# Optimization experiments

Measured on AMD Instinct MI355X. Metric: run time of the kernel, lower is better.

The kernel has to match this reference:

```python
import jax, jax.numpy as jnp
import numpy as np

DIM = 1024
NUM_HEADS = 16
HEAD_DIM = DIM // NUM_HEADS
SCALE = HEAD_DIM ** -0.5


def setup_inputs() -> dict:
    key = jax.random.key(0)
    ks = jax.random.split(key, 11)
    B, N, M = 8, 1024, 1024
    s = DIM ** -0.5  # init scale for weights
    return {
        "x": jax.random.normal(ks[0], (B, N, DIM), jnp.float32),
        "context": jax.random.normal(ks[1], (B, M, DIM), jnp.float32),
        "Wq": jax.random.normal(ks[2], (DIM, DIM), jnp.float32) * s,
        "bq": jax.random.normal(ks[3], (DIM,), jnp.float32) * 0.01,
        "Wk": jax.random.normal(ks[4], (DIM, DIM), jnp.float32) * s,
        "bk": jax.random.normal(ks[5], (DIM,), jnp.float32) * 0.01,
        "Wv": jax.random.normal(ks[6], (DIM, DIM), jnp.float32) * s,
        "bv": jax.random.normal(ks[7], (DIM,), jnp.float32) * 0.01,
        "Wo": jax.random.normal(ks[8], (DIM, DIM), jnp.float32) * s,
        "bo": jax.random.normal(ks[9], (DIM,), jnp.float32) * 0.01,
    }


def reference(x, context, Wq, bq, Wk, bk, Wv, bv, Wo, bo):
    B, N, _ = x.shape
    M = context.shape[1]
    # Linear projections (torch Linear: x @ W.T + b; here W stored as [in, out])
    q = x @ Wq + bq            # [B, N, DIM]
    k = context @ Wk + bk      # [B, M, DIM]
    v = context @ Wv + bv      # [B, M, DIM]
    # split heads: b n (h d) -> b h n d
    q = q.reshape(B, N, NUM_HEADS, HEAD_DIM).transpose(0, 2, 1, 3)
    k = k.reshape(B, M, NUM_HEADS, HEAD_DIM).transpose(0, 2, 1, 3)
    v = v.reshape(B, M, NUM_HEADS, HEAD_DIM).transpose(0, 2, 1, 3)
    dots = jnp.einsum('bhnd,bhmd->bhnm', q, k) * SCALE
    attn = jax.nn.softmax(dots, axis=-1)
    out = jnp.einsum('bhnm,bhmd->bhnd', attn, v)   # [B, H, N, d]
    out = out.transpose(0, 2, 1, 3).reshape(B, N, DIM)  # b h n d -> b n (h d)
    return out @ Wo + bo
```

## Files before the change

kernel.cpp:

```cpp
#include <hip/hip_runtime.h>

typedef unsigned short u16;
typedef __attribute__((ext_vector_type(8))) short bf16x8;
typedef __attribute__((ext_vector_type(4))) float f32x4;
typedef __attribute__((ext_vector_type(16))) float f32x16;
typedef __attribute__((ext_vector_type(4))) unsigned u32x4;

#define MFMA16 __builtin_amdgcn_mfma_f32_16x16x32_bf16
#define MFMA32 __builtin_amdgcn_mfma_f32_32x32x16_bf16

__device__ __forceinline__ u16 f2b(float f) {
  unsigned u = __builtin_bit_cast(unsigned, f);
  u = (u + 0x7fffu + ((u >> 16) & 1u)) >> 16;
  return (u16)u;
}

__device__ __forceinline__ void gload_lds16(const u16* g, u16* l) {
  __builtin_amdgcn_global_load_lds((const __attribute__((address_space(1))) void*)g,
                                   (__attribute__((address_space(3))) void*)l, 16, 0, 0);
}

__global__ void prep(const float* __restrict__ x, const float* __restrict__ ctx,
                     u16* __restrict__ xb, u16* __restrict__ cb,
                     const float* __restrict__ w0, const float* __restrict__ w1,
                     const float* __restrict__ w2, const float* __restrict__ w3,
                     u16* __restrict__ o0, u16* __restrict__ o1,
                     u16* __restrict__ o2, u16* __restrict__ o3) {
  __shared__ float t[64][65];
  const int z = blockIdx.z;
  const int tid = threadIdx.x;
  if (z < 2) {
    int i = blockIdx.x * blockDim.x + tid;
    const float* in = z ? ctx : x;
    u16* out = z ? cb : xb;
    float4 v = reinterpret_cast<const float4*>(in)[i];
    reinterpret_cast<ushort4*>(out)[i] = make_ushort4(f2b(v.x), f2b(v.y), f2b(v.z), f2b(v.w));
    return;
  }
  const int id = blockIdx.x;
  if (id >= 1024) return;
  const int wsel = id >> 8;
  const float* src = wsel == 0 ? w0 : wsel == 1 ? w1 : wsel == 2 ? w2 : w3;
  u16* dst = wsel == 0 ? o0 : wsel == 1 ? o1 : wsel == 2 ? o2 : o3;
  const int r0 = ((id >> 4) & 15) * 64, c0 = (id & 15) * 64;
  #pragma unroll
  for (int it = 0; it < 4; ++it) {
    int row = it * 16 + (tid >> 4);
    int col = (tid & 15) * 4;
    float4 v = *reinterpret_cast<const float4*>(&src[(size_t)(r0 + row) * 1024 + c0 + col]);
    t[row][col] = v.x; t[row][col + 1] = v.y; t[row][col + 2] = v.z; t[row][col + 3] = v.w;
  }
  __syncthreads();
  #pragma unroll
  for (int it = 0; it < 2; ++it) {
    int c = it * 32 + (tid >> 3);
    int r8 = (tid & 7) * 8;
    u16 tmp[8];
    #pragma unroll
    for (int k = 0; k < 8; ++k) tmp[k] = f2b(t[r8 + k][c]);
    uint4 pk;
    pk.x = (unsigned)tmp[0] | ((unsigned)tmp[1] << 16);
    pk.y = (unsigned)tmp[2] | ((unsigned)tmp[3] << 16);
    pk.z = (unsigned)tmp[4] | ((unsigned)tmp[5] << 16);
    pk.w = (unsigned)tmp[6] | ((unsigned)tmp[7] << 16);
    *reinterpret_cast<uint4*>(&dst[(size_t)(c0 + c) * 1024 + r0 + r8]) = pk;
  }
}

__global__ __launch_bounds__(512, 2) void gemm_qkv256(
    const u16* __restrict__ xb, const u16* __restrict__ cb,
    const u16* __restrict__ Wqt, const u16* __restrict__ Wkt, const u16* __restrict__ Wvt,
    const float* __restrict__ bq, const float* __restrict__ bk, const float* __restrict__ bv,
    u16* __restrict__ Qb, u16* __restrict__ Kf, u16* __restrict__ Vf) {
  __shared__ u16 smem[65536];
  const int tid = threadIdx.x;
  const int lane = tid & 63;
  const int w = tid >> 6;
  const int wr = w >> 2, wc = w & 3;
  const int l16 = lane & 15, g = (lane >> 4) & 3;
  const int z = blockIdx.z;
  const u16* Ain = z == 0 ? xb : cb;
  const u16* W = z == 0 ? Wqt : z == 1 ? Wkt : Wvt;
  const float* bias = z == 0 ? bq : z == 1 ? bk : bv;
  const int brow = blockIdx.x * 256, bcol = blockIdx.y * 256;

  int aoff[4], boff[4];
  #pragma unroll
  for (int it = 0; it < 4; ++it) {
    const int c = it * 512 + tid;
    const int kk = ((c >> 6) & 1) * 32 + ((c >> 4) & 3) * 8;
    const int arow = (c >> 10) * 128 + ((c >> 7) & 7) * 16 + (c & 15);
    aoff[it] = (brow + arow) * 1024 + kk;
    const int bcolc = (c >> 9) * 64 + ((c >> 7) & 3) * 16 + (c & 15);
    boff[it] = (bcol + bcolc) * 1024 + kk;
  }
  auto stage = [&](int buf, int t) {
    u16* db = smem + buf * 32768;
    #pragma unroll
    for (int it = 0; it < 4; ++it)
      gload_lds16(&Ain[(size_t)(aoff[it] + t * 64)], db + (it * 512 + w * 64) * 8);
    #pragma unroll
    for (int it = 0; it < 4; ++it)
      gload_lds16(&W[(size_t)(boff[it] + t * 64)], db + 16384 + (it * 512 + w * 64) * 8);
  };

  f32x4 acc[8][4] = {};
  stage(0, 0);
  stage(1, 1);
  asm volatile("s_waitcnt vmcnt(8)" ::: "memory");
  __builtin_amdgcn_sched_barrier(0);
  __builtin_amdgcn_s_barrier();
  __builtin_amdgcn_sched_barrier(0);

  for (int t = 0; t < 16; ++t) {
    const int cur = t & 1;
    const u16* As = smem + cur * 32768;
    const u16* Bs = As + 16384;
    bf16x8 bfr[2][4];
    #pragma unroll
    for (int ks = 0; ks < 2; ++ks)
      #pragma unroll
      for (int ni = 0; ni < 4; ++ni)
        bfr[ks][ni] = *reinterpret_cast<const bf16x8*>(&Bs[(wc * 512 + ni * 128 + ks * 64 + lane) * 8]);
    __builtin_amdgcn_s_setprio(1);
    #pragma unroll
    for (int mi = 0; mi < 8; ++mi) {
      bf16x8 a0 = *reinterpret_cast<const bf16x8*>(&As[(wr * 1024 + mi * 128 + lane) * 8]);
      bf16x8 a1 = *reinterpret_cast<const bf16x8*>(&As[(wr * 1024 + mi * 128 + 64 + lane) * 8]);
      #pragma unroll
      for (int ni = 0; ni < 4; ++ni)
        acc[mi][ni] = MFMA16(a1, bfr[1][ni], MFMA16(a0, bfr[0][ni], acc[mi][ni], 0, 0, 0), 0, 0, 0);
    }
    __builtin_amdgcn_s_setprio(0);
    __builtin_amdgcn_sched_barrier(0);
    __builtin_amdgcn_s_barrier();
    __builtin_amdgcn_sched_barrier(0);
    if (t < 14) {
      stage(cur, t + 2);
      asm volatile("s_waitcnt vmcnt(8)" ::: "memory");
    } else {
      asm volatile("s_waitcnt vmcnt(0)" ::: "memory");
    }
    __builtin_amdgcn_sched_barrier(0);
    __builtin_amdgcn_s_barrier();
    __builtin_amdgcn_sched_barrier(0);
  }

  u16* T = smem + w * 4608;
  float bz[4];
  #pragma unroll
  for (int ni = 0; ni < 4; ++ni) bz[ni] = bias[bcol + wc * 64 + ni * 16 + l16];
  const float CS = 0.125f * 1.44269504089f;
  const int h = (bcol + wc * 64) >> 6;
  #pragma unroll
  for (int p = 0; p < 2; ++p) {
    if (z < 2) {
      #pragma unroll
      for (int mi4 = 0; mi4 < 4; ++mi4)
        #pragma unroll
        for (int ni = 0; ni < 4; ++ni) {
          f32x4 v = acc[p * 4 + mi4][ni];
          #pragma unroll
          for (int j = 0; j < 4; ++j) {
            float val = v[j] + bz[ni];
            if (z == 0) val *= CS;
            T[(mi4 * 16 + g * 4 + j) * 72 + ni * 16 + l16] = f2b(val);
          }
        }
      if (z == 0) {
        #pragma unroll
        for (int it = 0; it < 8; ++it) {
          const int rl = it * 8 + (lane >> 3), c8 = (lane & 7) * 8;
          bf16x8 val = *reinterpret_cast<const bf16x8*>(&T[rl * 72 + c8]);
          *reinterpret_cast<bf16x8*>(
              &Qb[(size_t)(brow + wr * 128 + p * 64 + rl) * 1024 + bcol + wc * 64 + c8]) = val;
        }
      } else {
        #pragma unroll
        for (int it = 0; it < 8; ++it) {
          const int rl = it * 8 + (lane >> 3), c8 = (lane & 7) * 8;
          bf16x8 val = *reinterpret_cast<const bf16x8*>(&T[rl * 72 + c8]);
          const int m = brow + wr * 128 + p * 64 + rl;
          const int bb = m >> 10, kt = (m & 1023) >> 6;
          const int chunk = (c8 >> 4) * 128 + ((m & 63) >> 5) * 64 + ((c8 >> 3) & 1) * 32 + (m & 31);
          *reinterpret_cast<bf16x8*>(&Kf[(((size_t)(bb * 16 + h)) * 16 + kt) * 4096 + chunk * 8]) = val;
        }
      }
    } else {
      #pragma unroll
      for (int mi4 = 0; mi4 < 4; ++mi4)
        #pragma unroll
        for (int ni = 0; ni < 4; ++ni) {
          f32x4 v = acc[p * 4 + mi4][ni];
          #pragma unroll
          for (int j = 0; j < 4; ++j)
            T[(ni * 16 + l16) * 72 + mi4 * 16 + g * 4 + j] = f2b(v[j] + bz[ni]);
        }
      #pragma unroll
      for (int it = 0; it < 8; ++it) {
        const int d = it * 8 + (lane >> 3), m8 = (lane & 7) * 8;
        bf16x8 val = *reinterpret_cast<const bf16x8*>(&T[d * 72 + m8]);
        const int m = brow + wr * 128 + p * 64 + m8;
        const int bb = m >> 10, kt = (m & 1023) >> 6;
        const int chunk = (m8 >> 4) * 128 + (d >> 5) * 64 + ((m8 >> 3) & 1) * 32 + (d & 31);
        *reinterpret_cast<bf16x8*>(&Vf[(((size_t)(bb * 16 + h)) * 16 + kt) * 4096 + chunk * 8]) = val;
      }
    }
  }
}

__device__ __forceinline__ void gemm_core(const u16* __restrict__ A, const u16* __restrict__ Wt,
                                          f32x4 (&acc)[4][4], int brow, int bcol,
                                          u16* __restrict__ smem) {
  const int tid = threadIdx.x;
  const int lane = tid & 63;
  const int w = tid >> 6;
  const int wr = w >> 1, wc = w & 1;
  const int l16 = lane & 15, g = lane >> 4;

  auto stage = [&](int buf, int kt) {
    #pragma unroll
    for (int it = 0; it < 4; ++it) {
      int c = it * 256 + tid;
      int row = (c >> 2) & 127;
      int ks = c >> 9;
      int k8 = c & 3;
      const size_t gofs = (size_t)kt * 64 + ks * 32 + k8 * 8;
      gload_lds16(&A[(size_t)(brow + row) * 1024 + gofs],
                  &smem[buf * 8192 + (it * 256 + w * 64) * 8]);
      gload_lds16(&Wt[(size_t)(bcol + row) * 1024 + gofs],
                  &smem[16384 + buf * 8192 + (it * 256 + w * 64) * 8]);
    }
  };

  stage(0, 0);
  __syncthreads();
  int cur = 0;
  for (int kt = 0; kt < 16; ++kt) {
    if (kt < 15) stage(cur ^ 1, kt + 1);
    const u16* As = &smem[cur * 8192];
    const u16* Bs = &smem[16384 + cur * 8192];
    #pragma unroll
    for (int ks = 0; ks < 2; ++ks) {
      bf16x8 a[4], b[4];
      const int kb = ks * 4096 + g * 8;
      #pragma unroll
      for (int mi = 0; mi < 4; ++mi)
        a[mi] = *reinterpret_cast<const bf16x8*>(&As[kb + (wr * 64 + mi * 16 + l16) * 32]);
      #pragma unroll
      for (int ni = 0; ni < 4; ++ni)
        b[ni] = *reinterpret_cast<const bf16x8*>(&Bs[kb + (wc * 64 + ni * 16 + l16) * 32]);
      #pragma unroll
      for (int mi = 0; mi < 4; ++mi)
        #pragma unroll
        for (int ni = 0; ni < 4; ++ni)
          acc[mi][ni] = MFMA16(a[mi], b[ni], acc[mi][ni], 0, 0, 0);
    }
    __syncthreads();
    cur ^= 1;
  }
}

__global__ __launch_bounds__(256, 2) void gemm_o(const u16* __restrict__ A, const u16* __restrict__ Wt,
                                                 const float* __restrict__ bias, float* __restrict__ outp) {
  __shared__ u16 smem[32768];
  const int brow = blockIdx.x * 128, bcol = blockIdx.y * 128;
  f32x4 acc[4][4] = {};
  gemm_core(A, Wt, acc, brow, bcol, smem);
  const int lane = threadIdx.x & 63;
  const int w = threadIdx.x >> 6;
  const int wr = w >> 1, wc = w & 1;
  const int l16 = lane & 15, g = lane >> 4;
  #pragma unroll
  for (int ni = 0; ni < 4; ++ni) {
    const int col = bcol + wc * 64 + ni * 16 + l16;
    const float bz = bias[col];
    #pragma unroll
    for (int mi = 0; mi < 4; ++mi) {
      const int r0 = brow + wr * 64 + mi * 16 + g * 4;
      f32x4 v = acc[mi][ni];
      #pragma unroll
      for (int j = 0; j < 4; ++j) outp[(size_t)(r0 + j) * 1024 + col] = v[j] + bz;
    }
  }
}

__global__ __launch_bounds__(256, 2) void attn2(const u16* __restrict__ Q, const u16* __restrict__ Kf,
                                                const u16* __restrict__ Vf, u16* __restrict__ AO) {
  __shared__ u16 Ks[2][64 * 64];
  __shared__ u16 Vs[2][64 * 64];
  const int tid = threadIdx.x, lane = tid & 63, w = tid >> 6;
  const int l32 = lane & 31, u = lane >> 5;
  const int id = blockIdx.x;
  const int v = (id & 7) * 128 + (id >> 3);
  const int qt = v & 7, h = (v >> 3) & 15, b = v >> 7;
  const int q0 = qt * 128 + w * 32;

  bf16x8 qf[4];
  {
    const u16* qp = &Q[(size_t)(b * 1024 + q0 + l32) * 1024 + h * 64 + u * 8];
    #pragma unroll
    for (int m = 0; m < 4; ++m) qf[m] = *reinterpret_cast<const bf16x8*>(qp + m * 16);
  }

  f32x16 o0 = {}, o1 = {};
  float lr = 0.f;

  const u16* Kbh = Kf + (size_t)(b * 16 + h) * 65536;
  const u16* Vbh = Vf + (size_t)(b * 16 + h) * 65536;

  auto stage = [&](int buf, int kt) {
    #pragma unroll
    for (int it = 0; it < 2; ++it) {
      const int c = (it * 256 + tid) * 8;
      gload_lds16(&Kbh[kt * 4096 + c], &Ks[buf][(it * 256 + w * 64) * 8]);
      gload_lds16(&Vbh[kt * 4096 + c], &Vs[buf][(it * 256 + w * 64) * 8]);
    }
  };

  stage(0, 0);
  __syncthreads();
  int cur = 0;

  for (int kt = 0; kt < 16; ++kt) {
    if (kt < 15) stage(cur ^ 1, kt + 1);

    f32x16 s0 = {}, s1 = {};
    __builtin_amdgcn_s_setprio(1);
    #pragma unroll
    for (int m = 0; m < 4; ++m) {
      bf16x8 k0 = *reinterpret_cast<const bf16x8*>(&Ks[cur][m * 1024 + lane * 8]);
      bf16x8 k1 = *reinterpret_cast<const bf16x8*>(&Ks[cur][m * 1024 + 512 + lane * 8]);
      s0 = MFMA32(k0, qf[m], s0, 0, 0, 0);
      s1 = MFMA32(k1, qf[m], s1, 0, 0, 0);
    }
    __builtin_amdgcn_s_setprio(0);

    unsigned W0[8], W1[8];
    #pragma unroll
    for (int j = 0; j < 8; ++j) {
      const int r = 4 * (j >> 1) + 2 * (j & 1);
      float pa0 = __builtin_amdgcn_exp2f(s0[r]);
      float pb0 = __builtin_amdgcn_exp2f(s0[r + 1]);
      float pa1 = __builtin_amdgcn_exp2f(s1[r]);
      float pb1 = __builtin_amdgcn_exp2f(s1[r + 1]);
      lr += (pa0 + pb0) + (pa1 + pb1);
      asm("v_cvt_pk_bf16_f32 %0, %1, %2" : "=v"(W0[j]) : "v"(pa0), "v"(pb0));
      asm("v_cvt_pk_bf16_f32 %0, %1, %2" : "=v"(W1[j]) : "v"(pa1), "v"(pb1));
    }

    unsigned paw[4][4];
    #pragma unroll
    for (int ks = 0; ks < 4; ++ks) {
      const int ksl = ks & 1;
      #pragma unroll
      for (int p = 0; p < 2; ++p) {
        unsigned x = (ks < 2) ? W0[4 * ksl + p] : W1[4 * ksl + p];
        unsigned y = (ks < 2) ? W0[4 * ksl + 2 + p] : W1[4 * ksl + 2 + p];
        asm("v_permlane32_swap_b32 %0, %1" : "+v"(x), "+v"(y));
        paw[ks][p] = x;
        paw[ks][2 + p] = y;
      }
    }

    __builtin_amdgcn_s_setprio(1);
    #pragma unroll
    for (int ks = 0; ks < 4; ++ks) {
      bf16x8 pa = __builtin_bit_cast(bf16x8, u32x4{paw[ks][0], paw[ks][1], paw[ks][2], paw[ks][3]});
      bf16x8 v0 = *reinterpret_cast<const bf16x8*>(&Vs[cur][ks * 1024 + lane * 8]);
      bf16x8 v1 = *reinterpret_cast<const bf16x8*>(&Vs[cur][ks * 1024 + 512 + lane * 8]);
      o0 = MFMA32(pa, v0, o0, 0, 0, 0);
      o1 = MFMA32(pa, v1, o1, 0, 0, 0);
    }
    __builtin_amdgcn_s_setprio(0);

    __syncthreads();
    cur ^= 1;
  }

  float sum = lr + __shfl_xor(lr, 32);
  float rinv = 1.0f / sum;
  u16* aop = &AO[(size_t)(b * 1024 + q0) * 1024 + h * 64 + l32];
  #pragma unroll
  for (int r = 0; r < 16; ++r) {
    const int ql = (r & 3) + 8 * (r >> 2) + 4 * u;
    int ri_i = __builtin_amdgcn_ds_bpermute((ql + (u << 5)) << 2, __builtin_bit_cast(int, rinv));
    float ri = __builtin_bit_cast(float, ri_i);
    aop[(size_t)ql * 1024] = f2b(o0[r] * ri);
    aop[(size_t)ql * 1024 + 32] = f2b(o1[r] * ri);
  }
}

extern "C" void kernel_launch(void* const* d_in, const int* in_sizes, int n_in,
                              void* d_out, int out_size, void* d_ws, size_t ws_size,
                              hipStream_t stream) {
  const float* x   = (const float*)d_in[0];
  const float* ctx = (const float*)d_in[1];
  const float* Wq  = (const float*)d_in[2];
  const float* bq  = (const float*)d_in[3];
  const float* Wk  = (const float*)d_in[4];
  const float* bk  = (const float*)d_in[5];
  const float* Wv  = (const float*)d_in[6];
  const float* bv  = (const float*)d_in[7];
  const float* Wo  = (const float*)d_in[8];
  const float* bo  = (const float*)d_in[9];
  float* out = (float*)d_out;
  char* ws = (char*)d_ws;

  u16* xb  = (u16*)(ws + (size_t)0);
  u16* cb  = (u16*)(ws + ((size_t)16 << 20));
  u16* Qb  = (u16*)(ws + ((size_t)32 << 20));
  u16* Kf  = (u16*)(ws + ((size_t)48 << 20));
  u16* Vf  = (u16*)(ws + ((size_t)64 << 20));
  u16* Wqt = (u16*)(ws + ((size_t)80 << 20));
  u16* Wkt = (u16*)(ws + ((size_t)82 << 20));
  u16* Wvt = (u16*)(ws + ((size_t)84 << 20));
  u16* Wot = (u16*)(ws + ((size_t)86 << 20));

  prep<<<dim3(8192, 1, 3), 256, 0, stream>>>(x, ctx, xb, cb, Wq, Wk, Wv, Wo, Wqt, Wkt, Wvt, Wot);
  gemm_qkv256<<<dim3(32, 4, 3), 512, 0, stream>>>(xb, cb, Wqt, Wkt, Wvt, bq, bk, bv, Qb, Kf, Vf);
  attn2<<<dim3(1024), 256, 0, stream>>>(Qb, Kf, Vf, xb );
  gemm_o<<<dim3(64, 8), 256, 0, stream>>>(xb, Wot, bo, out);
}
```

Before: 172.5 us.

## Split QKV GEMM K-step into four quadrant phases with finer-grained prefetch

```diff
diff --git a/kernel.cpp b/kernel.cpp
--- a/kernel.cpp
+++ b/kernel.cpp
@@ -67,6 +67,35 @@
   }
 }
 
+#define PHASE(BUF, HA, HB, STAGE, VM)                                            \
+  do {                                                                           \
+    const u16* Ab = smem + (BUF) * 32768 + (HA) * 8192;                          \
+    const u16* Bb = smem + (BUF) * 32768 + 16384 + (HB) * 8192;                  \
+    bf16x8 afr[4][2], bfr[2][2];                                                 \
+    _Pragma("unroll") for (int mil = 0; mil < 4; ++mil)                          \
+      _Pragma("unroll") for (int ks = 0; ks < 2; ++ks)                           \
+        afr[mil][ks] = *(const bf16x8*)&Ab[(wr * 512 + mil * 128 + ks * 64 + lane) * 8]; \
+    _Pragma("unroll") for (int nil = 0; nil < 2; ++nil)                          \
+      _Pragma("unroll") for (int ks = 0; ks < 2; ++ks)                           \
+        bfr[nil][ks] = *(const bf16x8*)&Bb[(wc * 256 + nil * 128 + ks * 64 + lane) * 8]; \
+    STAGE;                                                                       \
+    asm volatile("s_waitcnt vmcnt(" #VM ")" ::: "memory");                       \
+    __builtin_amdgcn_sched_barrier(0);                                           \
+    __builtin_amdgcn_s_barrier();                                                \
+    asm volatile("s_waitcnt lgkmcnt(0)" ::: "memory");                           \
+    __builtin_amdgcn_sched_barrier(0);                                           \
+    __builtin_amdgcn_s_setprio(1);                                               \
+    _Pragma("unroll") for (int mil = 0; mil < 4; ++mil)                          \
+      _Pragma("unroll") for (int nil = 0; nil < 2; ++nil)                        \
+        acc[(HA) * 4 + mil][(HB) * 2 + nil] =                                    \
+            MFMA16(afr[mil][1], bfr[nil][1],                                     \
+                   MFMA16(afr[mil][0], bfr[nil][0],                              \
+                          acc[(HA) * 4 + mil][(HB) * 2 + nil], 0, 0, 0), 0, 0, 0); \
+    __builtin_amdgcn_s_setprio(0);                                               \
+    __builtin_amdgcn_sched_barrier(0);                                           \
+    __builtin_amdgcn_s_barrier();                                                \
+  } while (0)
+
 __global__ __launch_bounds__(512, 2) void gemm_qkv256(
     const u16* __restrict__ xb, const u16* __restrict__ cb,
     const u16* __restrict__ Wqt, const u16* __restrict__ Wkt, const u16* __restrict__ Wvt,
@@ -78,73 +107,59 @@
   const int w = tid >> 6;
   const int wr = w >> 2, wc = w & 3;
   const int l16 = lane & 15, g = (lane >> 4) & 3;
-  const int z = blockIdx.z;
+  const int id = blockIdx.x;
+  const int v = (id & 7) * 48 + (id >> 3);
+  const int bx = v & 31, by = (v >> 5) & 3, z = v >> 7;
   const u16* Ain = z == 0 ? xb : cb;
   const u16* W = z == 0 ? Wqt : z == 1 ? Wkt : Wvt;
   const float* bias = z == 0 ? bq : z == 1 ? bk : bv;
-  const int brow = blockIdx.x * 256, bcol = blockIdx.y * 256;
-
-  int aoff[4], boff[4];
-  #pragma unroll
-  for (int it = 0; it < 4; ++it) {
+  const int brow = bx * 256, bcol = by * 256;
+
+  int aoff0[2], boff0[2];
+  #pragma unroll
+  for (int it = 0; it < 2; ++it) {
     const int c = it * 512 + tid;
     const int kk = ((c >> 6) & 1) * 32 + ((c >> 4) & 3) * 8;
-    const int arow = (c >> 10) * 128 + ((c >> 7) & 7) * 16 + (c & 15);
-    aoff[it] = (brow + arow) * 1024 + kk;
-    const int bcolc = (c >> 9) * 64 + ((c >> 7) & 3) * 16 + (c & 15);
-    boff[it] = (bcol + bcolc) * 1024 + kk;
-  }
-  auto stage = [&](int buf, int t) {
-    u16* db = smem + buf * 32768;
-    #pragma unroll
-    for (int it = 0; it < 4; ++it)
-      gload_lds16(&Ain[(size_t)(aoff[it] + t * 64)], db + (it * 512 + w * 64) * 8);
-    #pragma unroll
-    for (int it = 0; it < 4; ++it)
-      gload_lds16(&W[(size_t)(boff[it] + t * 64)], db + 16384 + (it * 512 + w * 64) * 8);
+    const int arow = ((c >> 9) & 1) * 128 + ((c >> 7) & 3) * 16 + (c & 15);
+    aoff0[it] = (brow + arow) * 1024 + kk;
+    const int bcolc = (c >> 8) * 64 + ((c >> 7) & 1) * 16 + (c & 15);
+    boff0[it] = (bcol + bcolc) * 1024 + kk;
+  }
+  auto stageA = [&](int buf, int h, int kt) {
+    u16* db = smem + buf * 32768 + h * 8192;
+    #pragma unroll
+    for (int it = 0; it < 2; ++it)
+      gload_lds16(&Ain[(size_t)(aoff0[it] + h * 65536 + kt * 64)], db + (it * 512 + w * 64) * 8);
   };
+  auto stageB = [&](int buf, int h, int kt) {
+    u16* db = smem + buf * 32768 + 16384 + h * 8192;
+    #pragma unroll
+    for (int it = 0; it < 2; ++it)
+      gload_lds16(&W[(size_t)(boff0[it] + h * 32768 + kt * 64)], db + (it * 512 + w * 64) * 8);
+  };
 
   f32x4 acc[8][4] = {};
-  stage(0, 0);
-  stage(1, 1);
+  stageA(0, 0, 0); stageB(0, 0, 0); stageB(0, 1, 0); stageA(0, 1, 0);
+  stageA(1, 0, 1); stageB(1, 0, 1);
   asm volatile("s_waitcnt vmcnt(8)" ::: "memory");
   __builtin_amdgcn_sched_barrier(0);
   __builtin_amdgcn_s_barrier();
-  __builtin_amdgcn_sched_barrier(0);
-
-  for (int t = 0; t < 16; ++t) {
-    const int cur = t & 1;
-    const u16* As = smem + cur * 32768;
-    const u16* Bs = As + 16384;
-    bf16x8 bfr[2][4];
-    #pragma unroll
-    for (int ks = 0; ks < 2; ++ks)
-      #pragma unroll
-      for (int ni = 0; ni < 4; ++ni)
-        bfr[ks][ni] = *reinterpret_cast<const bf16x8*>(&Bs[(wc * 512 + ni * 128 + ks * 64 + lane) * 8]);
-    __builtin_amdgcn_s_setprio(1);
-    #pragma unroll
-    for (int mi = 0; mi < 8; ++mi) {
-      bf16x8 a0 = *reinterpret_cast<const bf16x8*>(&As[(wr * 1024 + mi * 128 + lane) * 8]);
-      bf16x8 a1 = *reinterpret_cast<const bf16x8*>(&As[(wr * 1024 + mi * 128 + 64 + lane) * 8]);
-      #pragma unroll
-      for (int ni = 0; ni < 4; ++ni)
-        acc[mi][ni] = MFMA16(a1, bfr[1][ni], MFMA16(a0, bfr[0][ni], acc[mi][ni], 0, 0, 0), 0, 0, 0);
-    }
-    __builtin_amdgcn_s_setprio(0);
-    __builtin_amdgcn_sched_barrier(0);
-    __builtin_amdgcn_s_barrier();
-    __builtin_amdgcn_sched_barrier(0);
-    if (t < 14) {
-      stage(cur, t + 2);
-      asm volatile("s_waitcnt vmcnt(8)" ::: "memory");
-    } else {
-      asm volatile("s_waitcnt vmcnt(0)" ::: "memory");
-    }
-    __builtin_amdgcn_sched_barrier(0);
-    __builtin_amdgcn_s_barrier();
-    __builtin_amdgcn_sched_barrier(0);
-  }
+
+  for (int t = 0; t < 14; ++t) {
+    const int buf = t & 1;
+    PHASE(buf, 0, 0, stageB(buf ^ 1, 1, t + 1), 8);
+    PHASE(buf, 0, 1, stageA(buf ^ 1, 1, t + 1), 8);
+    PHASE(buf, 1, 0, stageA(buf, 0, t + 2), 8);
+    PHASE(buf, 1, 1, stageB(buf, 0, t + 2), 8);
+  }
+  PHASE(0, 0, 0, stageB(1, 1, 15), 8);
+  PHASE(0, 0, 1, stageA(1, 1, 15), 8);
+  PHASE(0, 1, 0, ((void)0), 8);
+  PHASE(0, 1, 1, ((void)0), 4);
+  PHASE(1, 0, 0, ((void)0), 2);
+  PHASE(1, 0, 1, ((void)0), 0);
+  PHASE(1, 1, 0, ((void)0), 0);
+  PHASE(1, 1, 1, ((void)0), 0);
 
   u16* T = smem + w * 4608;
   float bz[4];
@@ -159,10 +174,10 @@
       for (int mi4 = 0; mi4 < 4; ++mi4)
         #pragma unroll
         for (int ni = 0; ni < 4; ++ni) {
-          f32x4 v = acc[p * 4 + mi4][ni];
+          f32x4 vv = acc[p * 4 + mi4][ni];
           #pragma unroll
           for (int j = 0; j < 4; ++j) {
-            float val = v[j] + bz[ni];
+            float val = vv[j] + bz[ni];
             if (z == 0) val *= CS;
             T[(mi4 * 16 + g * 4 + j) * 72 + ni * 16 + l16] = f2b(val);
           }
@@ -191,10 +206,10 @@
       for (int mi4 = 0; mi4 < 4; ++mi4)
         #pragma unroll
         for (int ni = 0; ni < 4; ++ni) {
-          f32x4 v = acc[p * 4 + mi4][ni];
+          f32x4 vv = acc[p * 4 + mi4][ni];
           #pragma unroll
           for (int j = 0; j < 4; ++j)
-            T[(ni * 16 + l16) * 72 + mi4 * 16 + g * 4 + j] = f2b(v[j] + bz[ni]);
+            T[(ni * 16 + l16) * 72 + mi4 * 16 + g * 4 + j] = f2b(vv[j] + bz[ni]);
         }
       #pragma unroll
       for (int it = 0; it < 8; ++it) {
@@ -418,7 +433,7 @@
   u16* Wot = (u16*)(ws + ((size_t)86 << 20));
 
   prep<<<dim3(8192, 1, 3), 256, 0, stream>>>(x, ctx, xb, cb, Wq, Wk, Wv, Wo, Wqt, Wkt, Wvt, Wot);
-  gemm_qkv256<<<dim3(32, 4, 3), 512, 0, stream>>>(xb, cb, Wqt, Wkt, Wvt, bq, bk, bv, Qb, Kf, Vf);
+  gemm_qkv256<<<dim3(384), 512, 0, stream>>>(xb, cb, Wqt, Wkt, Wvt, bq, bk, bv, Qb, Kf, Vf);
   attn2<<<dim3(1024), 256, 0, stream>>>(Qb, Kf, Vf, xb );
   gemm_o<<<dim3(64, 8), 256, 0, stream>>>(xb, Wot, bo, out);
 }
```

After: 166.5 us. 1.04x faster.

## Restructure QKV GEMM pipeline to issue next-tile loads before compute with one barrier

Applied to the files above, without the earlier changes.

```diff
diff --git a/kernel.cpp b/kernel.cpp
--- a/kernel.cpp
+++ b/kernel.cpp
@@ -80,7 +80,7 @@
   const int l16 = lane & 15, g = (lane >> 4) & 3;
   const int z = blockIdx.z;
   const u16* Ain = z == 0 ? xb : cb;
-  const u16* W = z == 0 ? Wqt : z == 1 ? Wkt : Wvt;
+  const u16* Wt = z == 0 ? Wqt : z == 1 ? Wkt : Wvt;
   const float* bias = z == 0 ? bq : z == 1 ? bk : bv;
   const int brow = blockIdx.x * 256, bcol = blockIdx.y * 256;
 
@@ -88,62 +88,56 @@
   #pragma unroll
   for (int it = 0; it < 4; ++it) {
     const int c = it * 512 + tid;
-    const int kk = ((c >> 6) & 1) * 32 + ((c >> 4) & 3) * 8;
-    const int arow = (c >> 10) * 128 + ((c >> 7) & 7) * 16 + (c & 15);
+    const int l = c & 63;
+    const int kk = (c >> 10) * 32 + ((l >> 4) & 3) * 8;
+    const int arow = ((c >> 9) & 1) * 128 + ((c >> 6) & 7) * 16 + (l & 15);
     aoff[it] = (brow + arow) * 1024 + kk;
-    const int bcolc = (c >> 9) * 64 + ((c >> 7) & 3) * 16 + (c & 15);
+    const int bcolc = ((c >> 8) & 3) * 64 + ((c >> 6) & 3) * 16 + (l & 15);
     boff[it] = (bcol + bcolc) * 1024 + kk;
   }
-  auto stage = [&](int buf, int t) {
-    u16* db = smem + buf * 32768;
+  auto stageAll = [&](int buf, int t) {
+    u16* da = smem + buf * 32768;
+    u16* db = da + 16384;
     #pragma unroll
     for (int it = 0; it < 4; ++it)
-      gload_lds16(&Ain[(size_t)(aoff[it] + t * 64)], db + (it * 512 + w * 64) * 8);
+      gload_lds16(&Ain[(size_t)(aoff[it] + t * 64)], da + (it * 512 + w * 64) * 8);
     #pragma unroll
     for (int it = 0; it < 4; ++it)
-      gload_lds16(&W[(size_t)(boff[it] + t * 64)], db + 16384 + (it * 512 + w * 64) * 8);
+      gload_lds16(&Wt[(size_t)(boff[it] + t * 64)], db + (it * 512 + w * 64) * 8);
   };
 
   f32x4 acc[8][4] = {};
-  stage(0, 0);
-  stage(1, 1);
-  asm volatile("s_waitcnt vmcnt(8)" ::: "memory");
+  stageAll(0, 0);
+  asm volatile("s_waitcnt vmcnt(0)" ::: "memory");
   __builtin_amdgcn_sched_barrier(0);
   __builtin_amdgcn_s_barrier();
-  __builtin_amdgcn_sched_barrier(0);
 
   for (int t = 0; t < 16; ++t) {
-    const int cur = t & 1;
-    const u16* As = smem + cur * 32768;
+    const int buf = t & 1;
+    if (t < 15) stageAll(buf ^ 1, t + 1);
+    __builtin_amdgcn_sched_barrier(0);
+    const u16* As = smem + buf * 32768;
     const u16* Bs = As + 16384;
-    bf16x8 bfr[2][4];
-    #pragma unroll
-    for (int ks = 0; ks < 2; ++ks)
-      #pragma unroll
-      for (int ni = 0; ni < 4; ++ni)
-        bfr[ks][ni] = *reinterpret_cast<const bf16x8*>(&Bs[(wc * 512 + ni * 128 + ks * 64 + lane) * 8]);
-    __builtin_amdgcn_s_setprio(1);
-    #pragma unroll
-    for (int mi = 0; mi < 8; ++mi) {
-      bf16x8 a0 = *reinterpret_cast<const bf16x8*>(&As[(wr * 1024 + mi * 128 + lane) * 8]);
-      bf16x8 a1 = *reinterpret_cast<const bf16x8*>(&As[(wr * 1024 + mi * 128 + 64 + lane) * 8]);
-      #pragma unroll
-      for (int ni = 0; ni < 4; ++ni)
-        acc[mi][ni] = MFMA16(a1, bfr[1][ni], MFMA16(a0, bfr[0][ni], acc[mi][ni], 0, 0, 0), 0, 0, 0);
-    }
-    __builtin_amdgcn_s_setprio(0);
+    #pragma unroll
+    for (int ks = 0; ks < 2; ++ks) {
+      bf16x8 afr[8], bfr[4];
+      #pragma unroll
+      for (int nil = 0; nil < 4; ++nil)
+        bfr[nil] = *reinterpret_cast<const bf16x8*>(&Bs[(ks * 1024 + wc * 256 + nil * 64 + lane) * 8]);
+      #pragma unroll
+      for (int mil = 0; mil < 8; ++mil)
+        afr[mil] = *reinterpret_cast<const bf16x8*>(&As[(ks * 1024 + wr * 512 + mil * 64 + lane) * 8]);
+      __builtin_amdgcn_s_setprio(1);
+      #pragma unroll
+      for (int mil = 0; mil < 8; ++mil)
+        #pragma unroll
+        for (int nil = 0; nil < 4; ++nil)
+          acc[mil][nil] = MFMA16(afr[mil], bfr[nil], acc[mil][nil], 0, 0, 0);
+      __builtin_amdgcn_s_setprio(0);
+    }
     __builtin_amdgcn_sched_barrier(0);
+    asm volatile("s_waitcnt vmcnt(0)" ::: "memory");
     __builtin_amdgcn_s_barrier();
-    __builtin_amdgcn_sched_barrier(0);
-    if (t < 14) {
-      stage(cur, t + 2);
-      asm volatile("s_waitcnt vmcnt(8)" ::: "memory");
-    } else {
-      asm volatile("s_waitcnt vmcnt(0)" ::: "memory");
-    }
-    __builtin_amdgcn_sched_barrier(0);
-    __builtin_amdgcn_s_barrier();
-    __builtin_amdgcn_sched_barrier(0);
   }
 
   u16* T = smem + w * 4608;
@@ -159,10 +153,10 @@
       for (int mi4 = 0; mi4 < 4; ++mi4)
         #pragma unroll
         for (int ni = 0; ni < 4; ++ni) {
-          f32x4 v = acc[p * 4 + mi4][ni];
+          f32x4 vv = acc[p * 4 + mi4][ni];
           #pragma unroll
           for (int j = 0; j < 4; ++j) {
-            float val = v[j] + bz[ni];
+            float val = vv[j] + bz[ni];
             if (z == 0) val *= CS;
             T[(mi4 * 16 + g * 4 + j) * 72 + ni * 16 + l16] = f2b(val);
           }
@@ -191,10 +185,10 @@
       for (int mi4 = 0; mi4 < 4; ++mi4)
         #pragma unroll
         for (int ni = 0; ni < 4; ++ni) {
-          f32x4 v = acc[p * 4 + mi4][ni];
+          f32x4 vv = acc[p * 4 + mi4][ni];
           #pragma unroll
           for (int j = 0; j < 4; ++j)
-            T[(ni * 16 + l16) * 72 + mi4 * 16 + g * 4 + j] = f2b(v[j] + bz[ni]);
+            T[(ni * 16 + l16) * 72 + mi4 * 16 + g * 4 + j] = f2b(vv[j] + bz[ni]);
         }
       #pragma unroll
       for (int it = 0; it < 8; ++it) {
```

Result: no change. 174.9 us (+1.4%).
